# Kernel tuning notes

Measured on AMD Instinct MI355X. Metric: run time of the kernel, lower is better.

## Reference

```python
import jax, jax.numpy as jnp
import numpy as np
from jax import lax

B, S, D_IN = 4, 4096, 1024
D_FAST, D_SLOW = 512, 512
Z_BIAS_FAST, Z_BIAS_SLOW = 2.0, -2.0


def _binop(q_i, q_j):
    a_i, b_i = q_i
    a_j, b_j = q_j
    return (a_i * a_j, a_j * b_i + b_j)


def parallel_scan(a, b):
    # h_t = a_t * h_{t-1} + b_t along seq axis (axis=1)
    _, h = lax.associative_scan(_binop, (a, b), axis=1)
    return h


def setup_inputs() -> dict:
    key = jax.random.key(0)
    ks = jax.random.split(key, 6)
    scale = 0.02
    x = jax.random.normal(ks[0], (B, S, D_IN), dtype=jnp.float32)
    W_zf = jax.random.normal(ks[1], (D_IN, D_FAST), dtype=jnp.float32) * scale
    b_zf = jnp.full((D_FAST,), Z_BIAS_FAST, dtype=jnp.float32)
    W_hf = jax.random.normal(ks[2], (D_IN, D_FAST), dtype=jnp.float32) * scale
    b_hf = jnp.zeros((D_FAST,), dtype=jnp.float32)
    W_zs = jax.random.normal(ks[3], (D_IN, D_SLOW), dtype=jnp.float32) * scale
    b_zs = jnp.full((D_SLOW,), Z_BIAS_SLOW, dtype=jnp.float32)
    W_hs = jax.random.normal(ks[4], (D_IN, D_SLOW), dtype=jnp.float32) * scale
    b_hs = jnp.zeros((D_SLOW,), dtype=jnp.float32)
    W_g = jax.random.normal(ks[5], (D_FAST + D_SLOW, D_FAST + D_SLOW), dtype=jnp.float32) * scale
    b_g = jnp.zeros((D_FAST + D_SLOW,), dtype=jnp.float32)
    return {"x": x, "W_zf": W_zf, "b_zf": b_zf, "W_hf": W_hf, "b_hf": b_hf,
            "W_zs": W_zs, "b_zs": b_zs, "W_hs": W_hs, "b_hs": b_hs,
            "W_g": W_g, "b_g": b_g}


def reference(x, W_zf, b_zf, W_hf, b_hf, W_zs, b_zs, W_hs, b_hs, W_g, b_g):
    # Fast compartment (coupling='output' => slow branch sees raw x)
    z_fast = jax.nn.sigmoid(jnp.einsum('bsd,df->bsf', x, W_zf) + b_zf)
    h_tilde_fast = jnp.einsum('bsd,df->bsf', x, W_hf) + b_hf
    h_fast = parallel_scan(1.0 - z_fast, z_fast * h_tilde_fast)

    # Slow compartment
    z_slow = jax.nn.sigmoid(jnp.einsum('bsd,df->bsf', x, W_zs) + b_zs)
    h_tilde_slow = jnp.einsum('bsd,df->bsf', x, W_hs) + b_hs
    h_slow = parallel_scan(1.0 - z_slow, z_slow * h_tilde_slow)

    h_combined = jnp.concatenate([h_fast, h_slow], axis=-1)  # (B, S, D_FAST+D_SLOW)
    gate = jax.nn.sigmoid(jnp.einsum('bsc,cd->bsd', h_combined, W_g) + b_g)
    return gate * h_combined
```

## Files before the change

kernel.cpp:

```cpp
#include <hip/hip_runtime.h>

#define BB 4
#define SS 4096
#define DIN 1024
#define DH 1024
#define PN 2048
#define MM (BB*SS)
#define NC 64
#define CL 64

typedef unsigned short ushort_t;
typedef __attribute__((ext_vector_type(8))) short bf16x8;
typedef __attribute__((ext_vector_type(4))) float f32x4;
typedef __attribute__((ext_vector_type(4))) unsigned short u16x4;

__device__ inline float bf2f(ushort_t u) {
    union { float f; unsigned int i; } v; v.i = ((unsigned int)u) << 16; return v.f;
}
__device__ inline ushort_t f2bf(float f) {
    union { float f; unsigned int i; } v; v.f = f;
    unsigned int r = v.i + 0x7fffu + ((v.i >> 16) & 1u);
    return (ushort_t)(r >> 16);
}
__device__ inline float sigmoidf_(float x) { return 1.0f / (1.0f + __expf(-x)); }

__device__ inline void load_lds16(const void* g, void* l) {
    __builtin_amdgcn_global_load_lds(
        (const __attribute__((address_space(1))) void*)g,
        (__attribute__((address_space(3))) void*)l, 16, 0, 0);
}

__device__ __forceinline__ bf16x8 ds128(const ushort_t* p) {
    bf16x8 r;
    asm volatile("ds_read_b128 %0, %1"
                 : "=v"(r)
                 : "v"((const __attribute__((address_space(3))) ushort_t*)p));
    return r;
}

__global__ void zero_out_kernel(float* out, int n) {
    int i = blockIdx.x * 256 + threadIdx.x;
    if (i < n) out[i] = 0.0f;
}

#define PREP_NBLK 17160
__global__ __launch_bounds__(256) void prep_kernel(
    const float* __restrict__ x,
    const float* __restrict__ Wzf, const float* __restrict__ Wzs,
    const float* __restrict__ Whf, const float* __restrict__ Whs,
    const float* __restrict__ Wg,
    const float* __restrict__ bzf, const float* __restrict__ bzs,
    const float* __restrict__ bhf, const float* __restrict__ bhs,
    ushort_t* __restrict__ WcatT, ushort_t* __restrict__ WgT,
    ushort_t* __restrict__ Xb, float* __restrict__ bcat)
{
    __shared__ ushort_t tile[64][65];
    const int bx = blockIdx.x, tid = threadIdx.x;

    if (bx < 768) {
        const float* src; ushort_t* dst; int srcN, t;
        if (bx < 512) {
            int wi = bx >> 7; t = bx & 127; srcN = 512;
            const float* S[4] = {Wzf, Wzs, Whf, Whs};
            src = S[wi];
            dst = WcatT + (size_t)(wi * 512) * DIN;
        } else {
            t = bx - 512; srcN = 1024; src = Wg; dst = WgT;
        }
        const int k0 = (t & 15) * 64, n0 = (t >> 4) * 64;
        const int tx = tid & 63, ty = tid >> 6;
        #pragma unroll
        for (int i = ty; i < 64; i += 4)
            tile[i][tx] = f2bf(src[(size_t)(k0 + i) * srcN + n0 + tx]);
        __syncthreads();
        #pragma unroll
        for (int i = ty; i < 64; i += 4)
            dst[(size_t)(n0 + i) * DIN + k0 + tx] = tile[tx][i];
    } else if (bx < 17152) {
        size_t i = ((size_t)(bx - 768) * 256 + tid) * 4;
        float4 v = *(const float4*)(x + i);
        u16x4 o;
        o.x = f2bf(v.x); o.y = f2bf(v.y); o.z = f2bf(v.z); o.w = f2bf(v.w);
        *(u16x4*)(Xb + i) = o;
    } else {
        int i = (bx - 17152) * 256 + tid;
        float v = (i < 512) ? bzf[i] : (i < 1024) ? bzs[i - 512]
                : (i < 1536) ? bhf[i - 1024] : bhs[i - 1536];
        bcat[i] = v;
    }
}

#define BARR __builtin_amdgcn_s_barrier()
#define WAITK { asm volatile("s_waitcnt lgkmcnt(0)"); __builtin_amdgcn_sched_barrier(0); }
#define VM4   { asm volatile("s_waitcnt vmcnt(4)");   __builtin_amdgcn_sched_barrier(0); }

#define STG_A(b, h, kt) { \
    _Pragma("unroll") \
    for (int j = 0; j < 2; j++) { \
        int c = wave * 2 + j; \
        load_lds16(Ablk + (size_t)((h) * 128 + c * 8) * lda + (kt) * 64 + laneAOff, \
                   &As[(b) * 16384 + (h) * 8192 + c * 512]); \
    } }

#define STG_B(b, h, kt) { \
    _Pragma("unroll") \
    for (int j = 0; j < 2; j++) { \
        int c = wave * 2 + j; \
        load_lds16(Bblk + (size_t)((h) * 128 + c * 8) * K + (kt) * 64 + laneBOff, \
                   &Bs[(b) * 16384 + (h) * 8192 + c * 512]); \
    } }

#define LOADA(b, qm) { \
    const ushort_t* p0 = &As[(b) * 16384 + (qm) * 8192 + arow0 + acol0]; \
    const ushort_t* p1 = &As[(b) * 16384 + (qm) * 8192 + arow0 + acol1]; \
    _Pragma("unroll") \
    for (int mt = 0; mt < 4; mt++) { \
        af[mt][0] = ds128(p0 + mt * 1024); \
        af[mt][1] = ds128(p1 + mt * 1024); \
    } }

#define LOADB(b, qn, bq) { \
    const ushort_t* p0 = &Bs[(b) * 16384 + (qn) * 8192 + brow0 + acol0]; \
    const ushort_t* p1 = &Bs[(b) * 16384 + (qn) * 8192 + brow0 + acol1]; \
    _Pragma("unroll") \
    for (int nt = 0; nt < 2; nt++) { \
        bq[nt][0] = ds128(p0 + nt * 1024); \
        bq[nt][1] = ds128(p1 + nt * 1024); \
    } }

#define MFMA16(qm, qn, bq) { \
    __builtin_amdgcn_s_setprio(1); \
    _Pragma("unroll") \
    for (int mt = 0; mt < 4; mt++) { \
        _Pragma("unroll") \
        for (int nt = 0; nt < 2; nt++) { \
            acc[qm][qn][mt][nt] = __builtin_amdgcn_mfma_f32_16x16x32_bf16( \
                af[mt][0], bq[nt][0], acc[qm][qn][mt][nt], 0, 0, 0); \
            acc[qm][qn][mt][nt] = __builtin_amdgcn_mfma_f32_16x16x32_bf16( \
                af[mt][1], bq[nt][1], acc[qm][qn][mt][nt], 0, 0, 0); \
        } } \
    __builtin_amdgcn_s_setprio(0); }

template <int EPI, int NB>
__global__ __launch_bounds__(512, 2) void gemm_kernel(
    const ushort_t* __restrict__ A, const ushort_t* __restrict__ Bt,
    int K, int lda,
    const float* __restrict__ bias,
    ushort_t* __restrict__ Zarr, ushort_t* __restrict__ Harr,
    const float* __restrict__ bg, const ushort_t* __restrict__ Hbf,
    float* __restrict__ Out)
{
    __shared__ alignas(16) ushort_t As[2 * 256 * 64];
    __shared__ alignas(16) ushort_t Bs[2 * 256 * 64];

    const int tid  = threadIdx.x;
    const int lane = tid & 63;
    const int wave = tid >> 6;
    const int wm   = wave & 1;
    const int wn   = wave >> 1;
    const int lrow = lane & 15;
    const int kgrp = lane >> 4;

    const int id  = blockIdx.x;
    const int xcd = id & 7;
    const int s   = id >> 3;
    const int mBase = (xcd + 8 * (s / NB)) * 256;
    const int nBase = (s % NB) * 256;

    f32x4 acc[2][2][4][2] = {};

    const ushort_t* Ablk = A  + (size_t)mBase * lda;
    const ushort_t* Bblk = Bt + (size_t)nBase * K;
    const int laneAOff = (lane >> 3) * lda + (((lane & 7) ^ (lane >> 3)) * 8);
    const int laneBOff = (lane >> 3) * K   + (((lane & 7) ^ (lane >> 3)) * 8);

    const int arow0 = (wm * 64 + lrow) * 64;
    const int brow0 = (wn * 32 + lrow) * 64;
    const int acol0 = ((kgrp    ) ^ (lrow & 7)) * 8;
    const int acol1 = ((4 + kgrp) ^ (lrow & 7)) * 8;

    const int NKT = K >> 6;
    const int NIT = NKT >> 1;

    bf16x8 af[4][2], bqA[2][2], bqB[2][2];

    STG_A(0, 0, 0); STG_B(0, 0, 0); STG_A(0, 1, 0); STG_B(0, 1, 0);
    STG_A(1, 0, 1); STG_B(1, 0, 1);
    VM4;
    BARR;

    for (int i = 0; i < NIT; i++) {
        const int kt1  = 2 * i + 1;
        const int ktn0 = (2 * i + 2) & (NKT - 1);
        const int ktn1 = (2 * i + 3) & (NKT - 1);

        LOADA(0, 0); LOADB(0, 0, bqA); STG_A(1, 1, kt1);
        BARR; WAITK; MFMA16(0, 0, bqA); BARR;
        LOADB(0, 1, bqB); STG_B(1, 1, kt1);
        BARR; WAITK; MFMA16(0, 1, bqB); BARR;
        LOADA(0, 1); STG_A(0, 0, ktn0);
        BARR; WAITK; MFMA16(1, 1, bqB); BARR;
        STG_B(0, 0, ktn0);
        BARR; MFMA16(1, 0, bqA); VM4; BARR;

        LOADA(1, 0); LOADB(1, 0, bqA); STG_B(0, 1, ktn0);
        BARR; WAITK; MFMA16(0, 0, bqA); BARR;
        LOADB(1, 1, bqB); STG_A(0, 1, ktn0);
        BARR; WAITK; MFMA16(0, 1, bqB); BARR;
        LOADA(1, 1); STG_A(1, 0, ktn1);
        BARR; WAITK; MFMA16(1, 1, bqB); BARR;
        STG_B(1, 0, ktn1);
        BARR; MFMA16(1, 0, bqA); VM4; BARR;
    }

    const int rquad = (lane >> 4) * 4;

    if (EPI == 0) {
        const bool isz = (nBase < DH);
        ushort_t* Dst  = isz ? Zarr : Harr;
        const int csub = isz ? 0 : DH;
        #pragma unroll
        for (int qm = 0; qm < 2; qm++)
        #pragma unroll
        for (int qn = 0; qn < 2; qn++)
        #pragma unroll
        for (int nt = 0; nt < 2; nt++) {
            int col  = nBase + qn * 128 + wn * 32 + nt * 16 + lrow;
            float bv = bias[col];
            int dcol = col - csub;
            #pragma unroll
            for (int mt = 0; mt < 4; mt++) {
                int row = mBase + qm * 128 + wm * 64 + mt * 16 + rquad;
                ushort_t* p = Dst + (size_t)row * DH + dcol;
                #pragma unroll
                for (int r = 0; r < 4; r++) {
                    float v = acc[qm][qn][mt][nt][r] + bv;
                    if (isz) v = sigmoidf_(v);
                    p[(size_t)r * DH] = f2bf(v);
                }
            }
        }
    } else {
        #pragma unroll
        for (int qm = 0; qm < 2; qm++)
        #pragma unroll
        for (int qn = 0; qn < 2; qn++)
        #pragma unroll
        for (int nt = 0; nt < 2; nt++) {
            int col  = nBase + qn * 128 + wn * 32 + nt * 16 + lrow;
            float bv = bg[col];
            #pragma unroll
            for (int mt = 0; mt < 4; mt++) {
                int row = mBase + qm * 128 + wm * 64 + mt * 16 + rquad;
                #pragma unroll
                for (int r = 0; r < 4; r++) {
                    float g = sigmoidf_(acc[qm][qn][mt][nt][r] + bv);
                    float h = bf2f(Hbf[(size_t)(row + r) * DH + col]);
                    Out[(size_t)(row + r) * DH + col] = g * h;
                }
            }
        }
    }
}

__global__ __launch_bounds__(256) void scan_chunk_agg(
    const ushort_t* __restrict__ Zarr, const ushort_t* __restrict__ Harr,
    float* __restrict__ Agg, float* __restrict__ Bagg)
{
    const int c4    = threadIdx.x * 4;
    const int chunk = blockIdx.x;
    const int b     = blockIdx.y;
    const size_t s0 = ((size_t)b * SS + (size_t)chunk * CL) * DH + c4;
    const ushort_t* Zp = Zarr + s0;
    const ushort_t* Hp = Harr + s0;

    float A0 = 1.0f, A1 = 1.0f, A2 = 1.0f, A3 = 1.0f;
    float B0 = 0.0f, B1 = 0.0f, B2 = 0.0f, B3 = 0.0f;
    #pragma unroll 8
    for (int t = 0; t < CL; t++) {
        u16x4 zv = *(const u16x4*)(Zp + (size_t)t * DH);
        u16x4 hv = *(const u16x4*)(Hp + (size_t)t * DH);
        float z0 = bf2f(zv.x), z1 = bf2f(zv.y), z2 = bf2f(zv.z), z3 = bf2f(zv.w);
        float h0 = bf2f(hv.x), h1 = bf2f(hv.y), h2 = bf2f(hv.z), h3 = bf2f(hv.w);
        A0 *= 1.0f - z0;  B0 = (1.0f - z0) * B0 + z0 * h0;
        A1 *= 1.0f - z1;  B1 = (1.0f - z1) * B1 + z1 * h1;
        A2 *= 1.0f - z2;  B2 = (1.0f - z2) * B2 + z2 * h2;
        A3 *= 1.0f - z3;  B3 = (1.0f - z3) * B3 + z3 * h3;
    }
    const size_t idx = ((size_t)(b * NC + chunk)) * DH + c4;
    *(float4*)(Agg  + idx) = make_float4(A0, A1, A2, A3);
    *(float4*)(Bagg + idx) = make_float4(B0, B1, B2, B3);
}

__global__ void scan_carry(const float* __restrict__ Agg, const float* __restrict__ Bagg,
                           float* __restrict__ Hinit)
{
    const int i = blockIdx.x * 256 + threadIdx.x;
    const int b = i >> 10, c = i & 1023;
    float h = 0.0f;
    for (int j = 0; j < NC; j++) {
        const size_t idx = ((size_t)(b * NC + j)) * DH + c;
        Hinit[idx] = h;
        h = Agg[idx] * h + Bagg[idx];
    }
}

__global__ __launch_bounds__(256) void scan_apply(
    const ushort_t* __restrict__ Zarr, ushort_t* Harr, const float* __restrict__ Hinit)
{
    const int c4    = threadIdx.x * 4;
    const int chunk = blockIdx.x;
    const int b     = blockIdx.y;
    const size_t s0 = ((size_t)b * SS + (size_t)chunk * CL) * DH + c4;
    const ushort_t* Zp = Zarr + s0;
    ushort_t*       Hp = Harr + s0;

    float4 hi = *(const float4*)(Hinit + ((size_t)(b * NC + chunk)) * DH + c4);
    float h0 = hi.x, h1 = hi.y, h2 = hi.z, h3 = hi.w;
    #pragma unroll 8
    for (int t = 0; t < CL; t++) {
        u16x4 zv = *(const u16x4*)(Zp + (size_t)t * DH);
        u16x4 hv = *(const u16x4*)(Hp + (size_t)t * DH);
        float z0 = bf2f(zv.x), z1 = bf2f(zv.y), z2 = bf2f(zv.z), z3 = bf2f(zv.w);
        float t0 = bf2f(hv.x), t1 = bf2f(hv.y), t2 = bf2f(hv.z), t3 = bf2f(hv.w);
        h0 = (1.0f - z0) * h0 + z0 * t0;
        h1 = (1.0f - z1) * h1 + z1 * t1;
        h2 = (1.0f - z2) * h2 + z2 * t2;
        h3 = (1.0f - z3) * h3 + z3 * t3;
        u16x4 o;
        o.x = f2bf(h0); o.y = f2bf(h1); o.z = f2bf(h2); o.w = f2bf(h3);
        *(u16x4*)(Hp + (size_t)t * DH) = o;
    }
}

extern "C" void kernel_launch(void* const* d_in, const int* in_sizes, int n_in,
                              void* d_out, int out_size, void* d_ws, size_t ws_size,
                              hipStream_t stream)
{
    const float* x   = (const float*)d_in[0];
    const float* Wzf = (const float*)d_in[1];
    const float* bzf = (const float*)d_in[2];
    const float* Whf = (const float*)d_in[3];
    const float* bhf = (const float*)d_in[4];
    const float* Wzs = (const float*)d_in[5];
    const float* bzs = (const float*)d_in[6];
    const float* Whs = (const float*)d_in[7];
    const float* bhs = (const float*)d_in[8];
    const float* Wg  = (const float*)d_in[9];
    const float* bg  = (const float*)d_in[10];

    const size_t NEED = (size_t)42 << 20;
    if (ws_size < NEED) {
        zero_out_kernel<<<(MM * DH + 255) / 256, 256, 0, stream>>>((float*)d_out, MM * DH);
        return;
    }

    char* ws = (char*)d_ws;
    ushort_t* WcatT = (ushort_t*)(ws);
    ushort_t* WgT   = (ushort_t*)(ws + ((size_t)4 << 20));
    float*    bcat  = (float*)   (ws + ((size_t)6 << 20));
    float*    Agg   = (float*)   (ws + ((size_t)6 << 20) + (64 << 10));
    float*    Bagg  = (float*)   (ws + ((size_t)7 << 20) + (64 << 10));
    float*    Hinit = (float*)   (ws + ((size_t)8 << 20) + (64 << 10));
    ushort_t* Harr  = (ushort_t*)(ws + ((size_t)10 << 20));

    ushort_t* Xb   = (ushort_t*)d_out;
    ushort_t* Zarr = Xb + (size_t)MM * DH;

    dim3 blk(256);

    prep_kernel<<<PREP_NBLK, blk, 0, stream>>>(
        x, Wzf, Wzs, Whf, Whs, Wg, bzf, bzs, bhf, bhs, WcatT, WgT, Xb, bcat);

    gemm_kernel<0, PN / 256><<<(MM / 256) * (PN / 256), dim3(512), 0, stream>>>(
        Xb, WcatT, DIN, DIN, bcat, Zarr, Harr, nullptr, nullptr, nullptr);

    scan_chunk_agg<<<dim3(NC, BB), blk, 0, stream>>>(Zarr, Harr, Agg, Bagg);
    scan_carry<<<16, 256, 0, stream>>>(Agg, Bagg, Hinit);
    scan_apply<<<dim3(NC, BB), blk, 0, stream>>>(Zarr, Harr, Hinit);

    gemm_kernel<1, DH / 256><<<(MM / 256) * (DH / 256), dim3(512), 0, stream>>>(
        Harr, WgT, DIN, DH, nullptr, nullptr, nullptr, bg, Harr,
        (float*)d_out);
}
```

Measured before the change: 306.9 us.

## Restructure GEMM LDS/global pipeline with partial lgkmcnt waits and deeper prefetch

Result: slower. 322.0 us (+4.9%).

```diff
diff --git a/kernel.cpp b/kernel.cpp
--- a/kernel.cpp
+++ b/kernel.cpp
@@ -91,8 +91,8 @@
 }
 
 #define BARR __builtin_amdgcn_s_barrier()
-#define WAITK { asm volatile("s_waitcnt lgkmcnt(0)"); __builtin_amdgcn_sched_barrier(0); }
-#define VM4   { asm volatile("s_waitcnt vmcnt(4)");   __builtin_amdgcn_sched_barrier(0); }
+#define LGKM(n) { asm volatile("s_waitcnt lgkmcnt(" #n ")"); __builtin_amdgcn_sched_barrier(0); }
+#define VM8   { asm volatile("s_waitcnt vmcnt(8)");   __builtin_amdgcn_sched_barrier(0); }
 
 #define STG_A(b, h, kt) { \
     _Pragma("unroll") \
@@ -128,17 +128,28 @@
         bq[nt][1] = ds128(p1 + nt * 1024); \
     } }
 
-#define MFMA16(qm, qn, bq) { \
+#define MTG(qm, qn, bq, mt) { \
+    acc[qm][qn][mt][0] = __builtin_amdgcn_mfma_f32_16x16x32_bf16( \
+        af[mt][0], bq[0][0], acc[qm][qn][mt][0], 0, 0, 0); \
+    acc[qm][qn][mt][0] = __builtin_amdgcn_mfma_f32_16x16x32_bf16( \
+        af[mt][1], bq[0][1], acc[qm][qn][mt][0], 0, 0, 0); \
+    acc[qm][qn][mt][1] = __builtin_amdgcn_mfma_f32_16x16x32_bf16( \
+        af[mt][0], bq[1][0], acc[qm][qn][mt][1], 0, 0, 0); \
+    acc[qm][qn][mt][1] = __builtin_amdgcn_mfma_f32_16x16x32_bf16( \
+        af[mt][1], bq[1][1], acc[qm][qn][mt][1], 0, 0, 0); }
+
+#define MFMA16W(qm, qn, bq) { \
     __builtin_amdgcn_s_setprio(1); \
-    _Pragma("unroll") \
-    for (int mt = 0; mt < 4; mt++) { \
-        _Pragma("unroll") \
-        for (int nt = 0; nt < 2; nt++) { \
-            acc[qm][qn][mt][nt] = __builtin_amdgcn_mfma_f32_16x16x32_bf16( \
-                af[mt][0], bq[nt][0], acc[qm][qn][mt][nt], 0, 0, 0); \
-            acc[qm][qn][mt][nt] = __builtin_amdgcn_mfma_f32_16x16x32_bf16( \
-                af[mt][1], bq[nt][1], acc[qm][qn][mt][nt], 0, 0, 0); \
-        } } \
+    LGKM(6); MTG(qm, qn, bq, 0); \
+    LGKM(4); MTG(qm, qn, bq, 1); \
+    LGKM(2); MTG(qm, qn, bq, 2); \
+    LGKM(0); MTG(qm, qn, bq, 3); \
+    __builtin_amdgcn_s_setprio(0); }
+
+#define MFMA16N(qm, qn, bq) { \
+    __builtin_amdgcn_s_setprio(1); \
+    MTG(qm, qn, bq, 0); MTG(qm, qn, bq, 1); \
+    MTG(qm, qn, bq, 2); MTG(qm, qn, bq, 3); \
     __builtin_amdgcn_s_setprio(0); }
 
 template <int EPI, int NB>
@@ -184,34 +195,54 @@
 
     bf16x8 af[4][2], bqA[2][2], bqB[2][2];
 
-    STG_A(0, 0, 0); STG_B(0, 0, 0); STG_A(0, 1, 0); STG_B(0, 1, 0);
-    STG_A(1, 0, 1); STG_B(1, 0, 1);
-    VM4;
+    STG_A(0, 0, 0); STG_B(0, 0, 0); STG_B(0, 1, 0); STG_A(0, 1, 0);
+    STG_A(1, 0, 1); STG_B(1, 0, 1); STG_B(1, 1, 1); STG_A(1, 1, 1);
+    VM8;
     BARR;
 
     for (int i = 0; i < NIT; i++) {
-        const int kt1  = 2 * i + 1;
         const int ktn0 = (2 * i + 2) & (NKT - 1);
         const int ktn1 = (2 * i + 3) & (NKT - 1);
 
-        LOADA(0, 0); LOADB(0, 0, bqA); STG_A(1, 1, kt1);
-        BARR; WAITK; MFMA16(0, 0, bqA); BARR;
-        LOADB(0, 1, bqB); STG_B(1, 1, kt1);
-        BARR; WAITK; MFMA16(0, 1, bqB); BARR;
-        LOADA(0, 1); STG_A(0, 0, ktn0);
-        BARR; WAITK; MFMA16(1, 1, bqB); BARR;
-        STG_B(0, 0, ktn0);
-        BARR; MFMA16(1, 0, bqA); VM4; BARR;
-
-        LOADA(1, 0); LOADB(1, 0, bqA); STG_B(0, 1, ktn0);
-        BARR; WAITK; MFMA16(0, 0, bqA); BARR;
-        LOADB(1, 1, bqB); STG_A(0, 1, ktn0);
-        BARR; WAITK; MFMA16(0, 1, bqB); BARR;
-        LOADA(1, 1); STG_A(1, 0, ktn1);
-        BARR; WAITK; MFMA16(1, 1, bqB); BARR;
-        STG_B(1, 0, ktn1);
-        BARR; MFMA16(1, 0, bqA); VM4; BARR;
-    }
+        LOADB(0, 0, bqA); LOADA(0, 0);
+        BARR;
+        MFMA16W(0, 0, bqA);
+        LOADB(0, 1, bqB);
+        BARR;
+        STG_A(0, 0, ktn0); STG_B(0, 0, ktn0);
+        BARR;
+        LGKM(0); MFMA16N(0, 1, bqB);
+        BARR;
+        LOADA(0, 1);
+        BARR;
+        MFMA16W(1, 1, bqB);
+        BARR;
+        STG_B(0, 1, ktn0); STG_A(0, 1, ktn0);
+        BARR;
+        MFMA16N(1, 0, bqA);
+        VM8;
+        BARR;
+
+        LOADB(1, 0, bqA); LOADA(1, 0);
+        BARR;
+        MFMA16W(0, 0, bqA);
+        LOADB(1, 1, bqB);
+        BARR;
+        STG_A(1, 0, ktn1); STG_B(1, 0, ktn1);
+        BARR;
+        LGKM(0); MFMA16N(0, 1, bqB);
+        BARR;
+        LOADA(1, 1);
+        BARR;
+        MFMA16W(1, 1, bqB);
+        BARR;
+        STG_B(1, 1, ktn1); STG_A(1, 1, ktn1);
+        BARR;
+        MFMA16N(1, 0, bqA);
+        VM8;
+        BARR;
+    }
+    LGKM(0);
 
     const int rquad = (lane >> 4) * 4;
 
```
